# Kernel optimization log

Hardware: AMD Instinct MI355X
Metric: run time of the kernel (lower is better)

## Reference

```python
import jax, jax.numpy as jnp
import numpy as np

N, M, DIM = 50000, 800000, 64
EPS_MSG = 1e-7
BN_EPS = 1e-5


def setup_inputs() -> dict:
    key = jax.random.key(0)
    ks = jax.random.split(key, 12)
    x = jax.random.normal(ks[0], (N, DIM), dtype=jnp.float32)
    edge_index = jax.random.randint(ks[1], (2, M), 0, N, dtype=jnp.int64)
    edge_attr = jax.random.normal(ks[2], (M, DIM), dtype=jnp.float32)
    s = 1.0 / np.sqrt(DIM)
    s2 = 1.0 / np.sqrt(2 * DIM)
    # 3 GENConv layers, each with MLP: Linear(dim,2dim)->BN->ReLU->Linear(2dim,dim)
    W1 = jax.random.uniform(ks[3], (3, DIM, 2 * DIM), jnp.float32, -s, s)
    b1 = jax.random.uniform(ks[4], (3, 2 * DIM), jnp.float32, -s, s)
    gamma = jnp.ones((3, 2 * DIM), jnp.float32)
    beta = jnp.zeros((3, 2 * DIM), jnp.float32)
    W2 = jax.random.uniform(ks[5], (3, 2 * DIM, DIM), jnp.float32, -s2, s2)
    b2 = jax.random.uniform(ks[6], (3, DIM), jnp.float32, -s2, s2)
    return {"x": x, "edge_index": edge_index, "edge_attr": edge_attr,
            "W1": W1, "b1": b1, "gamma": gamma, "beta": beta, "W2": W2, "b2": b2}


def _genconv(x, src, dst, edge_attr, W1, b1, g, be, W2, b2):
    n = x.shape[0]
    # message: relu(x_j + e) + eps   (per-edge)
    msg = jax.nn.relu(x[src] + edge_attr) + EPS_MSG  # [M, dim]
    # softmax aggregation (per-destination, per-channel), t=1.0
    mx = jax.ops.segment_max(msg, dst, num_segments=n)
    mx = jnp.where(jnp.isfinite(mx), mx, 0.0)  # empty segments
    e = jnp.exp(msg - mx[dst])
    ssum = jax.ops.segment_sum(e, dst, num_segments=n)
    alpha = e / jnp.maximum(ssum[dst], 1e-16)
    agg = jax.ops.segment_sum(msg * alpha, dst, num_segments=n)  # [N, dim]
    # residual then MLP: Linear -> BatchNorm(train) -> ReLU -> Linear
    h = agg + x
    h1 = h @ W1 + b1
    mu = h1.mean(axis=0)
    var = h1.var(axis=0)
    h1 = (h1 - mu) * jax.lax.rsqrt(var + BN_EPS) * g + be
    h1 = jax.nn.relu(h1)
    return h1 @ W2 + b2


def reference(x, edge_index, edge_attr, W1, b1, gamma, beta, W2, b2):
    src, dst = edge_index[0], edge_index[1]
    for i in range(3):
        x = _genconv(x, src, dst, edge_attr, W1[i], b1[i], gamma[i], beta[i], W2[i], b2[i])
    return x
```

## Files before the change

kernel.cpp:

```cpp
#include <hip/hip_runtime.h>

#define DIM 64
#define D2  128


__global__ void k_detect(const int* __restrict__ ei, int m, int* __restrict__ flag) {
  __shared__ int nz;
  int t = threadIdx.x;
  if (t == 0) nz = 0;
  __syncthreads();
  int lim = 4096;
  if (lim > m / 2) lim = m / 2;
  int any = 0;
  for (int i = t; i < lim; i += 256) any |= (ei[2 * i + 1] != 0);
  if (any) atomicOr(&nz, 1);
  __syncthreads();
  if (t == 0) flag[0] = nz ? 0 : 1;
}

__global__ void k_hist(const int* __restrict__ ei, int m, const int* __restrict__ flag,
                       int* __restrict__ cnt) {
  int i = blockIdx.x * 256 + threadIdx.x;
  if (i >= m) return;
  int f = flag[0];
  int d = f ? ei[2 * ((size_t)m + i)] : ei[(size_t)m + i];
  atomicAdd(&cnt[d], 1);
}

__global__ void k_scanA(const int* __restrict__ cnt, int* __restrict__ excl,
                        int* __restrict__ bsum, int n) {
  __shared__ int lds[256];
  int t = threadIdx.x;
  int i = blockIdx.x * 256 + t;
  int v = (i < n) ? cnt[i] : 0;
  lds[t] = v;
  __syncthreads();
  for (int off = 1; off < 256; off <<= 1) {
    int u = (t >= off) ? lds[t - off] : 0;
    __syncthreads();
    lds[t] += u;
    __syncthreads();
  }
  if (i < n) excl[i] = lds[t] - v;
  if (t == 255) bsum[blockIdx.x] = lds[255];
}

__global__ void k_scanB(const int* __restrict__ bsum, int* __restrict__ boff, int nb) {
  __shared__ int lds[256];
  int t = threadIdx.x;
  int v = (t < nb) ? bsum[t] : 0;
  lds[t] = v;
  __syncthreads();
  for (int off = 1; off < 256; off <<= 1) {
    int u = (t >= off) ? lds[t - off] : 0;
    __syncthreads();
    lds[t] += u;
    __syncthreads();
  }
  if (t < nb) boff[t] = lds[t] - v;
}

__global__ void k_scanC(const int* __restrict__ excl, const int* __restrict__ boff,
                        int* __restrict__ start, int* __restrict__ cursor, int n, int m) {
  int i = blockIdx.x * 256 + threadIdx.x;
  if (i < n) {
    int s = excl[i] + boff[i >> 8];
    start[i] = s;
    cursor[i] = s;
  }
  if (i == 0) start[n] = m;
}

__global__ void k_scatter(const int* __restrict__ ei, int m, const int* __restrict__ flag,
                          int* __restrict__ cursor, int2* __restrict__ sed) {
  int i = blockIdx.x * 256 + threadIdx.x;
  if (i >= m) return;
  int f = flag[0];
  int s, d;
  if (f) { s = ei[2 * (size_t)i]; d = ei[2 * ((size_t)m + i)]; }
  else   { s = ei[i];             d = ei[(size_t)m + i]; }
  int pos = atomicAdd(&cursor[d], 1);
  sed[pos] = make_int2(i, s);
}

__global__ void k_sortseg(int2* __restrict__ sed, const int* __restrict__ start, int n) {
  int v = blockIdx.x * 256 + threadIdx.x;
  if (v >= n) return;
  int s0 = start[v], s1 = start[v + 1];
  for (int p = s0 + 1; p < s1; p++) {
    int2 key = sed[p];
    int q = p - 1;
    while (q >= s0) {
      int2 t = sed[q];
      if (t.x <= key.x) break;
      sed[q + 1] = t;
      q--;
    }
    sed[q + 1] = key;
  }
}

__global__ __launch_bounds__(256) void k_agg(
    const float* __restrict__ x, const float* __restrict__ ea,
    const int2* __restrict__ sed, const int* __restrict__ start,
    float* __restrict__ h, int n) {
  int lane = threadIdx.x & 63;
  int node = blockIdx.x * 4 + (threadIdx.x >> 6);
  if (node >= n) return;
  int sub = lane >> 3;
  int cl = lane & 7;
  int s0 = start[node], s1 = start[node + 1];

  float mM[8], sS[8], wW[8];
#pragma unroll
  for (int c = 0; c < 8; c++) { mM[c] = 0.f; sS[c] = 0.f; wW[c] = 0.f; }

  for (int base = s0; base < s1; base += 64) {
    int cnt = s1 - base;
    if (cnt > 64) cnt = 64;
    long long edata = 0;
    if (lane < cnt) edata = *(const long long*)&sed[base + lane];
    int nIter = (cnt + 7) >> 3;
    for (int t = 0; t < nIter; t++) {
      int idx = 8 * t + sub;
      long long ed = __shfl(edata, idx, 64);
      if (idx < cnt) {
        int eid = (int)(ed & 0xffffffffLL);
        int src = (int)((unsigned long long)ed >> 32);
        const float* xr = &x[(size_t)src * DIM + cl * 8];
        const float* ar = &ea[(size_t)eid * DIM + cl * 8];
        float4 xa = *(const float4*)xr;
        float4 xb = *(const float4*)(xr + 4);
        float4 aa = *(const float4*)ar;
        float4 ab = *(const float4*)(ar + 4);
        float xv[8] = {xa.x, xa.y, xa.z, xa.w, xb.x, xb.y, xb.z, xb.w};
        float av[8] = {aa.x, aa.y, aa.z, aa.w, ab.x, ab.y, ab.z, ab.w};
#pragma unroll
        for (int c = 0; c < 8; c++) {
          float g = fmaxf(xv[c] + av[c], 0.f) + 1e-7f;
          float nm = fmaxf(mM[c], g);
          float sc = __expf(mM[c] - nm);
          float pv = __expf(g - nm);
          sS[c] = sS[c] * sc + pv;
          wW[c] = wW[c] * sc + g * pv;
          mM[c] = nm;
        }
      }
    }
  }

#pragma unroll
  for (int off = 8; off < 64; off <<= 1) {
#pragma unroll
    for (int c = 0; c < 8; c++) {
      float om = __shfl_xor(mM[c], off, 64);
      float os = __shfl_xor(sS[c], off, 64);
      float ow = __shfl_xor(wW[c], off, 64);
      float M = fmaxf(mM[c], om);
      float e1 = __expf(mM[c] - M), e2 = __expf(om - M);
      sS[c] = sS[c] * e1 + os * e2;
      wW[c] = wW[c] * e1 + ow * e2;
      mM[c] = M;
    }
  }

  if (sub == 0) {
    const float* xr = &x[(size_t)node * DIM + cl * 8];
    float4 xa = *(const float4*)xr;
    float4 xb = *(const float4*)(xr + 4);
    float xv[8] = {xa.x, xa.y, xa.z, xa.w, xb.x, xb.y, xb.z, xb.w};
    float o[8];
#pragma unroll
    for (int c = 0; c < 8; c++) o[c] = wW[c] / fmaxf(sS[c], 1e-16f) + xv[c];
    *(float4*)&h[(size_t)node * DIM + cl * 8] = make_float4(o[0], o[1], o[2], o[3]);
    *(float4*)&h[(size_t)node * DIM + cl * 8 + 4] = make_float4(o[4], o[5], o[6], o[7]);
  }
}

__global__ __launch_bounds__(256) void k_gemm1(
    const float* __restrict__ h, const float* __restrict__ W1,
    const float* __restrict__ b1, float* __restrict__ h1,
    float* __restrict__ ps, float* __restrict__ pq, int n) {
  __shared__ float ws[DIM * D2];
  __shared__ float hs[DIM][68];
  __shared__ float red[8][D2];
  int tid = threadIdx.x;
  int row0 = blockIdx.x * 64;
  const float4* w4 = (const float4*)W1;
  float4* ws4 = (float4*)ws;
#pragma unroll
  for (int i = 0; i < 8; i++) ws4[tid + 256 * i] = w4[tid + 256 * i];
  const float4* h4 = (const float4*)h;
#pragma unroll
  for (int i = 0; i < 4; i++) {
    int idx = tid + 256 * i;
    int r = idx & 63, dg = idx >> 6;
    int row = row0 + r;
    float4 v = make_float4(0.f, 0.f, 0.f, 0.f);
    if (row < n) v = h4[(size_t)row * 16 + dg];
    int c = dg * 4;
    hs[c + 0][r] = v.x; hs[c + 1][r] = v.y; hs[c + 2][r] = v.z; hs[c + 3][r] = v.w;
  }
  __syncthreads();

  int tc = tid & 31, tr = tid >> 5;
  float bb[4];
#pragma unroll
  for (int k = 0; k < 4; k++) bb[k] = b1[tc * 4 + k];
  float acc[8][4];
#pragma unroll
  for (int i = 0; i < 8; i++)
#pragma unroll
    for (int k = 0; k < 4; k++) acc[i][k] = bb[k];
#pragma unroll 4
  for (int d = 0; d < DIM; d++) {
    float4 wv = *(const float4*)&ws[d * D2 + tc * 4];
    float4 ha = *(const float4*)&hs[d][tr * 8];
    float4 hb = *(const float4*)&hs[d][tr * 8 + 4];
    float hr[8] = {ha.x, ha.y, ha.z, ha.w, hb.x, hb.y, hb.z, hb.w};
    float wk[4] = {wv.x, wv.y, wv.z, wv.w};
#pragma unroll
    for (int i = 0; i < 8; i++)
#pragma unroll
      for (int k = 0; k < 4; k++) acc[i][k] = fmaf(hr[i], wk[k], acc[i][k]);
  }
  float cs[4] = {0.f, 0.f, 0.f, 0.f}, cq[4] = {0.f, 0.f, 0.f, 0.f};
#pragma unroll
  for (int i = 0; i < 8; i++) {
    int row = row0 + tr * 8 + i;
    if (row < n) {
      ((float4*)h1)[(size_t)row * 32 + tc] =
          make_float4(acc[i][0], acc[i][1], acc[i][2], acc[i][3]);
#pragma unroll
      for (int k = 0; k < 4; k++) { cs[k] += acc[i][k]; cq[k] += acc[i][k] * acc[i][k]; }
    }
  }
  __syncthreads();
#pragma unroll
  for (int k = 0; k < 4; k++) red[tr][tc * 4 + k] = cs[k];
  __syncthreads();
  float asum = 0.f;
  if (tid < D2) {
#pragma unroll
    for (int r = 0; r < 8; r++) asum += red[r][tid];
  }
  __syncthreads();
#pragma unroll
  for (int k = 0; k < 4; k++) red[tr][tc * 4 + k] = cq[k];
  __syncthreads();
  if (tid < D2) {
    float bsumv = 0.f;
#pragma unroll
    for (int r = 0; r < 8; r++) bsumv += red[r][tid];
    ps[(size_t)tid * gridDim.x + blockIdx.x] = asum;
    pq[(size_t)tid * gridDim.x + blockIdx.x] = bsumv;
  }
}

__global__ __launch_bounds__(256) void k_stats(
    const float* __restrict__ ps, const float* __restrict__ pq,
    const float* __restrict__ gamma, const float* __restrict__ beta,
    float* __restrict__ ss, int rows, int n) {
  __shared__ float r0[256], r1[256];
  int j = blockIdx.x;
  int t = threadIdx.x;
  float a = 0.f, b = 0.f;
  for (int r = t; r < rows; r += 256) {
    a += ps[(size_t)j * rows + r];
    b += pq[(size_t)j * rows + r];
  }
  r0[t] = a; r1[t] = b;
  __syncthreads();
  for (int off = 128; off > 0; off >>= 1) {
    if (t < off) { r0[t] += r0[t + off]; r1[t] += r1[t + off]; }
    __syncthreads();
  }
  if (t == 0) {
    float mu = r0[0] / (float)n;
    float var = r1[0] / (float)n - mu * mu;
    float sc = gamma[j] * rsqrtf(var + 1e-5f);
    ss[j] = sc;
    ss[D2 + j] = beta[j] - mu * sc;
  }
}

__global__ __launch_bounds__(256) void k_gemm2(
    const float* __restrict__ h1, const float* __restrict__ W2,
    const float* __restrict__ b2, const float* __restrict__ ss,
    float* __restrict__ out, int n) {
  __shared__ float ws2[D2 * DIM];
  __shared__ float hs[D2][68];
  __shared__ float scS[D2], shS[D2];
  int tid = threadIdx.x;
  int row0 = blockIdx.x * 64;
  const float4* w4 = (const float4*)W2;
  float4* ws4 = (float4*)ws2;
#pragma unroll
  for (int i = 0; i < 8; i++) ws4[tid + 256 * i] = w4[tid + 256 * i];
  if (tid < D2) { scS[tid] = ss[tid]; shS[tid] = ss[D2 + tid]; }
  __syncthreads();
  const float4* h14 = (const float4*)h1;
#pragma unroll
  for (int i = 0; i < 8; i++) {
    int idx = tid + 256 * i;
    int r = idx & 63, cg = idx >> 6;
    int row = row0 + r;
    float4 v = make_float4(0.f, 0.f, 0.f, 0.f);
    if (row < n) v = h14[(size_t)row * 32 + cg];
    int c = cg * 4;
    hs[c + 0][r] = fmaxf(fmaf(v.x, scS[c + 0], shS[c + 0]), 0.f);
    hs[c + 1][r] = fmaxf(fmaf(v.y, scS[c + 1], shS[c + 1]), 0.f);
    hs[c + 2][r] = fmaxf(fmaf(v.z, scS[c + 2], shS[c + 2]), 0.f);
    hs[c + 3][r] = fmaxf(fmaf(v.w, scS[c + 3], shS[c + 3]), 0.f);
  }
  __syncthreads();
  int tc = tid & 15, tr = tid >> 4;
  float bb[4];
#pragma unroll
  for (int k = 0; k < 4; k++) bb[k] = b2[tc * 4 + k];
  float acc[4][4];
#pragma unroll
  for (int i = 0; i < 4; i++)
#pragma unroll
    for (int k = 0; k < 4; k++) acc[i][k] = bb[k];
#pragma unroll 4
  for (int d = 0; d < D2; d++) {
    float4 wv = *(const float4*)&ws2[d * DIM + tc * 4];
    float4 hv = *(const float4*)&hs[d][tr * 4];
    float hr[4] = {hv.x, hv.y, hv.z, hv.w};
    float wk[4] = {wv.x, wv.y, wv.z, wv.w};
#pragma unroll
    for (int i = 0; i < 4; i++)
#pragma unroll
      for (int k = 0; k < 4; k++) acc[i][k] = fmaf(hr[i], wk[k], acc[i][k]);
  }
#pragma unroll
  for (int i = 0; i < 4; i++) {
    int row = row0 + tr * 4 + i;
    if (row < n)
      ((float4*)out)[(size_t)row * 16 + tc] =
          make_float4(acc[i][0], acc[i][1], acc[i][2], acc[i][3]);
  }
}

extern "C" void kernel_launch(void* const* d_in, const int* in_sizes, int n_in,
                              void* d_out, int out_size, void* d_ws, size_t ws_size,
                              hipStream_t stream) {
  (void)n_in; (void)out_size; (void)ws_size;
  const float* x0    = (const float*)d_in[0];
  const int*   ei    = (const int*)d_in[1];
  const float* ea    = (const float*)d_in[2];
  const float* W1    = (const float*)d_in[3];
  const float* b1    = (const float*)d_in[4];
  const float* gamma = (const float*)d_in[5];
  const float* beta  = (const float*)d_in[6];
  const float* W2    = (const float*)d_in[7];
  const float* b2    = (const float*)d_in[8];
  float* out = (float*)d_out;

  int n = in_sizes[0] / DIM;
  int m = in_sizes[1] / 2;

  char* base = (char*)d_ws;
  size_t off = 0;
  auto alloc = [&](size_t bytes) -> void* {
    void* p = base + off;
    off += (bytes + 255) & ~(size_t)255;
    return p;
  };
  int*   cnt    = (int*)alloc((size_t)n * 4);
  int*   excl   = (int*)alloc((size_t)n * 4);
  int*   bsum   = (int*)alloc(256 * 4);
  int*   boff   = (int*)alloc(256 * 4);
  int*   start  = (int*)alloc((size_t)(n + 1) * 4);
  int*   cursor = (int*)alloc((size_t)n * 4);
  int*   flag   = (int*)alloc(256);
  int2*  sed    = (int2*)alloc((size_t)m * 8);
  float* h      = (float*)alloc((size_t)n * DIM * 4);
  float* h1     = (float*)alloc((size_t)n * D2 * 4);
  int tiles = (n + 63) / 64;
  float* ps = (float*)alloc((size_t)tiles * D2 * 4);
  float* pq = (float*)alloc((size_t)tiles * D2 * 4);
  float* ss = (float*)alloc(256 * 4);

  hipMemsetAsync(cnt, 0, (size_t)n * 4, stream);
  k_detect<<<1, 256, 0, stream>>>(ei, m, flag);
  int mg = (m + 255) / 256;
  int ng = (n + 255) / 256;
  k_hist<<<mg, 256, 0, stream>>>(ei, m, flag, cnt);
  k_scanA<<<ng, 256, 0, stream>>>(cnt, excl, bsum, n);
  k_scanB<<<1, 256, 0, stream>>>(bsum, boff, ng);
  k_scanC<<<ng, 256, 0, stream>>>(excl, boff, start, cursor, n, m);
  k_scatter<<<mg, 256, 0, stream>>>(ei, m, flag, cursor, sed);
  k_sortseg<<<ng, 256, 0, stream>>>(sed, start, n);

  for (int l = 0; l < 3; l++) {
    const float* xin = (l == 0) ? x0 : out;
    k_agg<<<(n + 3) / 4, 256, 0, stream>>>(xin, ea, sed, start, h, n);
    k_gemm1<<<tiles, 256, 0, stream>>>(h, W1 + (size_t)l * DIM * D2, b1 + (size_t)l * D2,
                                       h1, ps, pq, n);
    k_stats<<<D2, 256, 0, stream>>>(ps, pq, gamma + (size_t)l * D2, beta + (size_t)l * D2,
                                    ss, tiles, n);
    k_gemm2<<<tiles, 256, 0, stream>>>(h1, W2 + (size_t)l * D2 * DIM, b2 + (size_t)l * DIM,
                                       ss, out, n);
  }
}
```

Measured before the change: 744.2 us.

## Replace per-node insertion sort with in-wave bitonic sort and fuse scan kernels

Removes the separate per-destination insertion-sort kernel and instead sorts each 64-edge chunk by edge id with a wavefront bitonic sort inside the aggregation kernel, keeping summation order deterministic. The block-offset scan kernel is also merged into the final scan step, with each block reducing the preceding block sums itself. This saves two launches and the serial, divergent insertion sort, but adds shuffle work to every aggregation call across the three layers. Segments longer than 64 edges are only sorted within each chunk, not across the whole segment.

```diff
diff --git a/kernel.cpp b/kernel.cpp
--- a/kernel.cpp
+++ b/kernel.cpp
@@ -45,30 +45,28 @@
   if (t == 255) bsum[blockIdx.x] = lds[255];
 }
 
-__global__ void k_scanB(const int* __restrict__ bsum, int* __restrict__ boff, int nb) {
-  __shared__ int lds[256];
+__global__ void k_scanC(const int* __restrict__ excl, const int* __restrict__ bsum,
+                        int* __restrict__ start, int* __restrict__ cursor, int n, int m) {
+  __shared__ int red[256];
+  __shared__ int boffS;
   int t = threadIdx.x;
-  int v = (t < nb) ? bsum[t] : 0;
-  lds[t] = v;
-  __syncthreads();
-  for (int off = 1; off < 256; off <<= 1) {
-    int u = (t >= off) ? lds[t - off] : 0;
+  int acc = 0;
+  for (int i = t; i < blockIdx.x; i += 256) acc += bsum[i];
+  red[t] = acc;
+  __syncthreads();
+  for (int off = 128; off > 0; off >>= 1) {
+    if (t < off) red[t] += red[t + off];
     __syncthreads();
-    lds[t] += u;
-    __syncthreads();
-  }
-  if (t < nb) boff[t] = lds[t] - v;
-}
-
-__global__ void k_scanC(const int* __restrict__ excl, const int* __restrict__ boff,
-                        int* __restrict__ start, int* __restrict__ cursor, int n, int m) {
-  int i = blockIdx.x * 256 + threadIdx.x;
+  }
+  if (t == 0) boffS = red[0];
+  __syncthreads();
+  int i = blockIdx.x * 256 + t;
   if (i < n) {
-    int s = excl[i] + boff[i >> 8];
+    int s = excl[i] + boffS;
     start[i] = s;
     cursor[i] = s;
   }
-  if (i == 0) start[n] = m;
+  if (blockIdx.x == 0 && t == 0) start[n] = m;
 }
 
 __global__ void k_scatter(const int* __restrict__ ei, int m, const int* __restrict__ flag,
@@ -83,22 +81,6 @@
   sed[pos] = make_int2(i, s);
 }
 
-__global__ void k_sortseg(int2* __restrict__ sed, const int* __restrict__ start, int n) {
-  int v = blockIdx.x * 256 + threadIdx.x;
-  if (v >= n) return;
-  int s0 = start[v], s1 = start[v + 1];
-  for (int p = s0 + 1; p < s1; p++) {
-    int2 key = sed[p];
-    int q = p - 1;
-    while (q >= s0) {
-      int2 t = sed[q];
-      if (t.x <= key.x) break;
-      sed[q + 1] = t;
-      q--;
-    }
-    sed[q + 1] = key;
-  }
-}
 
 __global__ __launch_bounds__(256) void k_agg(
     const float* __restrict__ x, const float* __restrict__ ea,
@@ -118,15 +100,30 @@
   for (int base = s0; base < s1; base += 64) {
     int cnt = s1 - base;
     if (cnt > 64) cnt = 64;
-    long long edata = 0;
-    if (lane < cnt) edata = *(const long long*)&sed[base + lane];
+    long long key = 0x7fffffffffffffffLL;
+    if (lane < cnt) {
+      unsigned long long u = *(const unsigned long long*)&sed[base + lane];
+      key = (long long)((u << 32) | (u >> 32));
+    }
+#pragma unroll
+    for (int k = 2; k <= 64; k <<= 1) {
+#pragma unroll
+      for (int j = k >> 1; j > 0; j >>= 1) {
+        long long o = __shfl_xor(key, j, 64);
+        bool up = ((lane & k) == 0);
+        bool lo = ((lane & j) == 0);
+        long long mn = key < o ? key : o;
+        long long mx = key < o ? o : key;
+        key = (up == lo) ? mn : mx;
+      }
+    }
     int nIter = (cnt + 7) >> 3;
     for (int t = 0; t < nIter; t++) {
       int idx = 8 * t + sub;
-      long long ed = __shfl(edata, idx, 64);
+      long long ed = __shfl(key, idx, 64);
       if (idx < cnt) {
-        int eid = (int)(ed & 0xffffffffLL);
-        int src = (int)((unsigned long long)ed >> 32);
+        int eid = (int)((unsigned long long)ed >> 32);
+        int src = (int)(ed & 0xffffffffLL);
         const float* xr = &x[(size_t)src * DIM + cl * 8];
         const float* ar = &ea[(size_t)eid * DIM + cl * 8];
         float4 xa = *(const float4*)xr;
@@ -371,7 +368,6 @@
   int*   cnt    = (int*)alloc((size_t)n * 4);
   int*   excl   = (int*)alloc((size_t)n * 4);
   int*   bsum   = (int*)alloc(256 * 4);
-  int*   boff   = (int*)alloc(256 * 4);
   int*   start  = (int*)alloc((size_t)(n + 1) * 4);
   int*   cursor = (int*)alloc((size_t)n * 4);
   int*   flag   = (int*)alloc(256);
@@ -389,10 +385,8 @@
   int ng = (n + 255) / 256;
   k_hist<<<mg, 256, 0, stream>>>(ei, m, flag, cnt);
   k_scanA<<<ng, 256, 0, stream>>>(cnt, excl, bsum, n);
-  k_scanB<<<1, 256, 0, stream>>>(bsum, boff, ng);
-  k_scanC<<<ng, 256, 0, stream>>>(excl, boff, start, cursor, n, m);
+  k_scanC<<<ng, 256, 0, stream>>>(excl, bsum, start, cursor, n, m);
   k_scatter<<<mg, 256, 0, stream>>>(ei, m, flag, cursor, sed);
-  k_sortseg<<<ng, 256, 0, stream>>>(sed, start, n);
 
   for (int l = 0; l < 3; l++) {
     const float* xin = (l == 0) ? x0 : out;
```

Measured after the change: 756.9 us. About the same (+1.7%).
